# Optimization experiments

Measured on AMD Instinct MI355X. Metric: run time of the kernel, lower is better.

The kernel has to match this reference:

```python
import jax, jax.numpy as jnp
import numpy as np

BN_EPS = 1e-5


def _bn_relu(x, gamma, beta):
    # BatchNorm1d in train mode over (batch, spatial) per channel, then ReLU.
    mean = jnp.mean(x, axis=(0, 2), keepdims=True)
    var = jnp.var(x, axis=(0, 2), keepdims=True)
    xn = (x - mean) * jax.lax.rsqrt(var + BN_EPS)
    return jax.nn.relu(xn * gamma[None, :, None] + beta[None, :, None])


def setup_inputs() -> dict:
    key = jax.random.key(0)
    ks = jax.random.split(key, 12)
    B, d1, d2, n_p, n_g = 16, 128, 256, 8192, 2048
    d_cat, d_h, d_out = d1 + d2, 256, 128
    return {
        "feature1": jax.random.normal(ks[0], (B, d1, n_p), jnp.float32),
        "coord1": jax.random.normal(ks[1], (B, 3, n_p), jnp.float32),
        "feature2": jax.random.normal(ks[2], (B, d2, n_g), jnp.float32),
        "coord2": jax.random.normal(ks[3], (B, 3, n_g), jnp.float32),
        "W1": jax.random.normal(ks[4], (d_h, d_cat), jnp.float32) * 0.05,
        "b1": jax.random.normal(ks[5], (d_h,), jnp.float32) * 0.05,
        "gamma1": jnp.ones((d_h,), jnp.float32),
        "beta1": jnp.zeros((d_h,), jnp.float32),
        "W2": jax.random.normal(ks[6], (d_out, d_h), jnp.float32) * 0.05,
        "b2": jax.random.normal(ks[7], (d_out,), jnp.float32) * 0.05,
        "gamma2": jnp.ones((d_out,), jnp.float32),
        "beta2": jnp.zeros((d_out,), jnp.float32),
    }


def reference(feature1, coord1, feature2, coord2,
              W1, b1, gamma1, beta1, W2, b2, gamma2, beta2):
    c1 = coord1.transpose(0, 2, 1)      # [B, n_p, 3]
    c2 = coord2.transpose(0, 2, 1)      # [B, n_g, 3]
    f2 = feature2.transpose(0, 2, 1)    # [B, n_g, d2]

    # squared pairwise distances [B, n_p, n_g]
    d2sq = (jnp.sum(c1 * c1, -1)[:, :, None]
            + jnp.sum(c2 * c2, -1)[:, None, :]
            - 2.0 * jnp.einsum('bpd,bgd->bpg', c1, c2))

    # 3 nearest neighbors via top_k of negated distances (ascending distance)
    neg, idx = jax.lax.top_k(-d2sq, 3)
    dists = -neg                                     # [B, n_p, 3]
    recip = 1.0 / (dists + 1e-8)
    weight = recip / jnp.sum(recip, axis=-1, keepdims=True)

    gathered = jax.vmap(lambda f, i: f[i])(f2, idx)  # [B, n_p, 3, d2]
    interp = jnp.sum(gathered * weight[..., None], axis=2)  # [B, n_p, d2]

    feat = jnp.concatenate([feature1.transpose(0, 2, 1), interp], axis=-1)
    feat = feat.transpose(0, 2, 1)                   # [B, d1+d2, n_p]

    h = _bn_relu(jnp.einsum('oc,bcn->bon', W1, feat) + b1[None, :, None], gamma1, beta1)
    out = _bn_relu(jnp.einsum('oc,bcn->bon', W2, h) + b2[None, :, None], gamma2, beta2)
    return out
```

## Files before the change

kernel.cpp:

```cpp
#include <hip/hip_runtime.h>

#define BB   16
#define D1   128
#define D2   256
#define NP   8192
#define NG   2048
#define DC   384
#define DH   256
#define DO   128
#define NPTS (BB*NP)
#define KRANGE 4
#define KSLICE (NG/KRANGE)

typedef unsigned int u32;
typedef unsigned short u16;
typedef short v8s __attribute__((ext_vector_type(8)));
typedef float v4f __attribute__((ext_vector_type(4)));

__device__ __forceinline__ u16 f2bf(float f) {
  u32 u = __builtin_bit_cast(u32, f);
  return (u16)((u + 0x7FFFu + ((u >> 16) & 1u)) >> 16);
}
__device__ __forceinline__ float bf2f(u32 lo16) {
  return __builtin_bit_cast(float, lo16 << 16);
}

__device__ __forceinline__ void gload16(const void* g, void* s) {
  __builtin_amdgcn_global_load_lds((const __attribute__((address_space(1))) void*)g,
                                   (__attribute__((address_space(3))) void*)s, 16, 0, 0);
}

__global__ __launch_bounds__(256) void prepw_kernel(const float* __restrict__ W1,
                                                    const float* __restrict__ W2,
                                                    u16* __restrict__ W1s, u16* __restrict__ W2s) {
  int id = blockIdx.x * 256 + threadIdx.x;
  if (id < 12288) {
    int ks = id >> 11, rem = id & 2047, m = rem >> 3, blk = rem & 7;
    int k = ks * 64 + (blk ^ (m & 7)) * 8;
    const float* src = W1 + m * 384 + k;
    u32 a0 = (u32)f2bf(src[0]) | ((u32)f2bf(src[1]) << 16);
    u32 a1 = (u32)f2bf(src[2]) | ((u32)f2bf(src[3]) << 16);
    u32 a2 = (u32)f2bf(src[4]) | ((u32)f2bf(src[5]) << 16);
    u32 a3 = (u32)f2bf(src[6]) | ((u32)f2bf(src[7]) << 16);
    uint4 v; v.x=a0; v.y=a1; v.z=a2; v.w=a3;
    *(uint4*)((char*)W1s + (long)id * 16) = v;
  }
  int id2 = id - 12288;
  if (id2 >= 0 && id2 < 4096) {
    int ks = id2 >> 10, rem = id2 & 1023, m = rem >> 3, blk = rem & 7;
    int k = ks * 64 + (blk ^ (m & 7)) * 8;
    const float* src = W2 + m * 256 + k;
    u32 a0 = (u32)f2bf(src[0]) | ((u32)f2bf(src[1]) << 16);
    u32 a1 = (u32)f2bf(src[2]) | ((u32)f2bf(src[3]) << 16);
    u32 a2 = (u32)f2bf(src[4]) | ((u32)f2bf(src[5]) << 16);
    u32 a3 = (u32)f2bf(src[6]) | ((u32)f2bf(src[7]) << 16);
    uint4 v; v.x=a0; v.y=a1; v.z=a2; v.w=a3;
    *(uint4*)((char*)W2s + (long)id2 * 16) = v;
  }
}

__global__ __launch_bounds__(256) void tf2_kernel(const float* __restrict__ f2, u16* __restrict__ f2t) {
  __shared__ float tl[64 * 65];
  int b = blockIdx.z, t = threadIdx.x;
  int c0 = blockIdx.y * 64, g0 = blockIdx.x * 64;
  const float* src = f2 + ((long)b * 256 + c0) * 2048 + g0;
  for (int i = t; i < 4096; i += 256) {
    int c = i >> 6, g = i & 63;
    tl[c * 65 + g] = src[(long)c * 2048 + g];
  }
  __syncthreads();
  for (int i = t; i < 2048; i += 256) {
    int g = i >> 5, cp = i & 31;
    int c = cp * 2;
    u32 v = (u32)f2bf(tl[c * 65 + g]) | ((u32)f2bf(tl[(c + 1) * 65 + g]) << 16);
    *(u32*)((char*)f2t + (((long)b * 2048 + g0 + g) * 256 + c0 + c) * 2) = v;
  }
}

__global__ __launch_bounds__(256) void knn_part_kernel(const float* __restrict__ c1, const float* __restrict__ c2,
                                                       float* __restrict__ ktD, int* __restrict__ ktI) {
  __shared__ float4 sg[KSLICE];
  int b = blockIdx.z, r = blockIdx.y, t = threadIdx.x;
  int base = r * KSLICE;
  const float* c2b = c2 + (long)b * 3 * NG;
  for (int g = t; g < KSLICE; g += 256) {
    int gg = base + g;
    float x = c2b[gg], y = c2b[NG + gg], z = c2b[2 * NG + gg];
    float s2 = __fadd_rn(__fadd_rn(__fmul_rn(x, x), __fmul_rn(y, y)), __fmul_rn(z, z));
    sg[g] = make_float4(x, y, z, s2);
  }
  __syncthreads();
  int p = blockIdx.x * 256 + t;
  const float* c1b = c1 + (long)b * 3 * NP;
  float px = c1b[p], py = c1b[NP + p], pz = c1b[2 * NP + p];
  float s1 = __fadd_rn(__fadd_rn(__fmul_rn(px, px), __fmul_rn(py, py)), __fmul_rn(pz, pz));
  float t0 = 1e30f, t1 = 1e30f, t2v = 1e30f;
  int i0 = 0, i1 = 0, i2 = 0;
  for (int g0 = 0; g0 < KSLICE; g0 += 8) {
    u32 mask = 0;
    #pragma unroll
    for (int u = 0; u < 8; u++) {
      float4 q = sg[g0 + u];
      float dot = __fadd_rn(__fadd_rn(__fmul_rn(px, q.x), __fmul_rn(py, q.y)), __fmul_rn(pz, q.z));
      float du = __fsub_rn(__fadd_rn(s1, q.w), __fmul_rn(2.0f, dot));
      mask |= (du < t2v) ? (1u << u) : 0u;
    }
    while (mask) {
      int u = __builtin_ctz(mask);
      mask &= mask - 1;
      float4 q = sg[g0 + u];
      float dot = __fadd_rn(__fadd_rn(__fmul_rn(px, q.x), __fmul_rn(py, q.y)), __fmul_rn(pz, q.z));
      float dd = __fsub_rn(__fadd_rn(s1, q.w), __fmul_rn(2.0f, dot));
      if (dd < t2v) {
        int gi = base + g0 + u;
        if (dd < t1) {
          t2v = t1; i2 = i1;
          if (dd < t0) { t1 = t0; i1 = i0; t0 = dd; i0 = gi; }
          else         { t1 = dd; i1 = gi; }
        } else { t2v = dd; i2 = gi; }
      }
    }
  }
  long n = (long)b * NP + p;
  long o = (long)(r * 3) * NPTS + n;
  ktD[o] = t0; ktD[o + NPTS] = t1; ktD[o + 2 * (long)NPTS] = t2v;
  ktI[o] = i0; ktI[o + NPTS] = i1; ktI[o + 2 * (long)NPTS] = i2;
}

__global__ __launch_bounds__(256) void knn_merge_kernel(const float* __restrict__ ktD, const int* __restrict__ ktI,
                                                        int* __restrict__ ki, float* __restrict__ kw) {
  long n = (long)blockIdx.x * 256 + threadIdx.x;
  float t0 = 1e30f, t1 = 1e30f, t2v = 1e30f;
  int i0 = 0, i1 = 0, i2 = 0;
  #pragma unroll
  for (int e = 0; e < KRANGE * 3; e++) {
    float d = ktD[(long)e * NPTS + n];
    int gi = ktI[(long)e * NPTS + n];
    if (d < t2v) {
      if (d < t1) {
        t2v = t1; i2 = i1;
        if (d < t0) { t1 = t0; i1 = i0; t0 = d; i0 = gi; }
        else        { t1 = d;  i1 = gi; }
      } else { t2v = d; i2 = gi; }
    }
  }
  float r0 = __fdiv_rn(1.0f, __fadd_rn(t0, 1e-8f));
  float r1 = __fdiv_rn(1.0f, __fadd_rn(t1, 1e-8f));
  float r2 = __fdiv_rn(1.0f, __fadd_rn(t2v, 1e-8f));
  float rs = __fadd_rn(__fadd_rn(r0, r1), r2);
  long o = n * 3;
  ki[o] = i0; ki[o + 1] = i1; ki[o + 2] = i2;
  kw[o]     = __fdiv_rn(r0, rs);
  kw[o + 1] = __fdiv_rn(r1, rs);
  kw[o + 2] = __fdiv_rn(r2, rs);
}

__global__ __launch_bounds__(256) void interp_kernel(const float* __restrict__ f1, const u16* __restrict__ f2t,
                                                     const int* __restrict__ ki, const float* __restrict__ kw,
                                                     u16* __restrict__ feat) {
  __shared__ float tile[64 * 130];
  int b = blockIdx.y, t = threadIdx.x;
  long p0 = (long)blockIdx.x * 64;
  const float* f1b = f1 + (long)b * D1 * NP;
  for (int i = t; i < D1 * 64; i += 256) {
    int c = i >> 6, p = i & 63;
    tile[p * 130 + c] = f1b[(long)c * NP + p0 + p];
  }
  __syncthreads();
  int p = t >> 2, q = t & 3;
  long n = (long)b * NP + p0 + p;
  char* row = (char*)feat + n * 768;
  int sw = p & 7;
  #pragma unroll
  for (int g = 0; g < 4; g++) {
    int c = q * 32 + g * 8;
    u32 w0 = (u32)f2bf(tile[p*130 + c+0]) | ((u32)f2bf(tile[p*130 + c+1]) << 16);
    u32 w1 = (u32)f2bf(tile[p*130 + c+2]) | ((u32)f2bf(tile[p*130 + c+3]) << 16);
    u32 w2 = (u32)f2bf(tile[p*130 + c+4]) | ((u32)f2bf(tile[p*130 + c+5]) << 16);
    u32 w3 = (u32)f2bf(tile[p*130 + c+6]) | ((u32)f2bf(tile[p*130 + c+7]) << 16);
    uint4 v; v.x=w0; v.y=w1; v.z=w2; v.w=w3;
    int c6 = c >> 6, kblk = (c & 63) >> 3;
    *(uint4*)(row + c6 * 128 + ((kblk ^ sw) << 4)) = v;
  }
  long o = n * 3;
  int g0 = ki[o], g1 = ki[o + 1], g2 = ki[o + 2];
  float w0 = kw[o], w1 = kw[o + 1], w2 = kw[o + 2];
  const char* fb = (const char*)f2t + (long)b * NG * 512;
  const char* r0 = fb + (long)g0 * 512;
  const char* r1 = fb + (long)g1 * 512;
  const char* r2 = fb + (long)g2 * 512;
  #pragma unroll
  for (int g = 0; g < 8; g++) {
    int ci = q * 64 + g * 8;
    uint4 a0 = *(const uint4*)(r0 + ci * 2);
    uint4 a1 = *(const uint4*)(r1 + ci * 2);
    uint4 a2 = *(const uint4*)(r2 + ci * 2);
    const u32* pa0 = (const u32*)&a0;
    const u32* pa1 = (const u32*)&a1;
    const u32* pa2 = (const u32*)&a2;
    u32 outw[4];
    #pragma unroll
    for (int h = 0; h < 4; h++) {
      u32 x0 = pa0[h], x1 = pa1[h], x2 = pa2[h];
      float lo = w0 * bf2f(x0 & 0xffff) + w1 * bf2f(x1 & 0xffff) + w2 * bf2f(x2 & 0xffff);
      float hi = w0 * bf2f(x0 >> 16)    + w1 * bf2f(x1 >> 16)    + w2 * bf2f(x2 >> 16);
      outw[h] = (u32)f2bf(lo) | ((u32)f2bf(hi) << 16);
    }
    uint4 v; v.x=outw[0]; v.y=outw[1]; v.z=outw[2]; v.w=outw[3];
    int c = 128 + ci;
    int c6 = c >> 6, kblk = (c & 63) >> 3;
    *(uint4*)(row + c6 * 128 + ((kblk ^ sw) << 4)) = v;
  }
}

__device__ __forceinline__ void mfma_tile(const char* lds, int buf, int wm, int wn, int l, v4f acc[4][4]) {
  const char* A = lds + buf * 16384;
  const char* Bp = lds + 32768 + buf * 16384;
  int lm = l & 15, lk = l >> 4, l7 = l & 7;
  #pragma unroll
  for (int w32 = 0; w32 < 2; w32++) {
    v8s af[4], bfr[4];
    #pragma unroll
    for (int mf = 0; mf < 4; mf++)
      af[mf] = *(const v8s*)(A + (wm * 64 + mf * 16 + lm) * 128 + (((w32 * 4 + lk) ^ l7) << 4));
    #pragma unroll
    for (int nf = 0; nf < 4; nf++)
      bfr[nf] = *(const v8s*)(Bp + (wn * 64 + nf * 16 + lm) * 128 + (((w32 * 4 + lk) ^ l7) << 4));
    #pragma unroll
    for (int mf = 0; mf < 4; mf++)
      #pragma unroll
      for (int nf = 0; nf < 4; nf++)
        acc[mf][nf] = __builtin_amdgcn_mfma_f32_16x16x32_bf16(af[mf], bfr[nf], acc[mf][nf], 0, 0, 0);
  }
}

__global__ __launch_bounds__(256) void gemm1_kernel(const u16* __restrict__ W1s, const u16* __restrict__ feat,
                                                    const float* __restrict__ b1, u16* __restrict__ y1,
                                                    float* __restrict__ ps, float* __restrict__ pq) {
  __shared__ __attribute__((aligned(16))) char lds[65536];
  const int t = threadIdx.x, w = t >> 6, l = t & 63;
  const int wm = w >> 1, wn = w & 1;
  const int nb = blockIdx.y, mb = blockIdx.x;
  const long n0 = (long)nb * 128;
  const int m0 = mb * 128;
  v4f acc[4][4];
  #pragma unroll
  for (int i = 0; i < 4; i++)
    #pragma unroll
    for (int j = 0; j < 4; j++) { v4f z = {0.f,0.f,0.f,0.f}; acc[i][j] = z; }

  auto stage = [&](int ks, int buf) {
    const char* srcA = (const char*)W1s + ks * 32768 + (long)m0 * 128 + w * 4096 + l * 16;
    char* dstA = (char*)lds + buf * 16384 + w * 4096;
    #pragma unroll
    for (int i = 0; i < 4; i++) gload16(srcA + i * 1024, dstA + i * 1024);
    char* dstB = (char*)lds + 32768 + buf * 16384 + w * 4096;
    #pragma unroll
    for (int i = 0; i < 4; i++) {
      int a = w * 4096 + i * 1024 + l * 16;
      int n = a >> 7, r = a & 127;
      const char* srcB = (const char*)feat + (n0 + n) * 768 + ks * 128 + r;
      gload16(srcB, dstB + i * 1024);
    }
  };

  stage(0, 0);
  __syncthreads();
  int buf = 0;
  for (int ks = 0; ks < 6; ks++) {
    if (ks < 5) stage(ks + 1, buf ^ 1);
    mfma_tile(lds, buf, wm, wn, l, acc);
    __syncthreads();
    buf ^= 1;
  }

  const int lm = l & 15, lk = l >> 4;
  #pragma unroll
  for (int mf = 0; mf < 4; mf++) {
    int m = m0 + wm * 64 + mf * 16 + lk * 4;
    float bb0 = b1[m], bb1 = b1[m+1], bb2 = b1[m+2], bb3 = b1[m+3];
    #pragma unroll
    for (int nf = 0; nf < 4; nf++) {
      long n = n0 + wn * 64 + nf * 16 + lm;
      v4f v = acc[mf][nf];
      v[0] += bb0; v[1] += bb1; v[2] += bb2; v[3] += bb3;
      acc[mf][nf] = v;
      uint2 pk;
      pk.x = (u32)f2bf(v[0]) | ((u32)f2bf(v[1]) << 16);
      pk.y = (u32)f2bf(v[2]) | ((u32)f2bf(v[3]) << 16);
      *(uint2*)((char*)y1 + (n * 256 + m) * 2) = pk;
    }
  }
  #pragma unroll
  for (int mf = 0; mf < 4; mf++) {
    #pragma unroll
    for (int j = 0; j < 4; j++) {
      float s = 0.f, q = 0.f;
      #pragma unroll
      for (int nf = 0; nf < 4; nf++) { float v = acc[mf][nf][j]; s += v; q += v * v; }
      #pragma unroll
      for (int mask = 1; mask <= 8; mask <<= 1) { s += __shfl_xor(s, mask); q += __shfl_xor(q, mask); }
      if (lm == 0) {
        int m = m0 + wm * 64 + mf * 16 + lk * 4 + j;
        int col = nb * 2 + wn;
        ps[(long)m * 2048 + col] = s;
        pq[(long)m * 2048 + col] = q;
      }
    }
  }
}

__global__ __launch_bounds__(256) void stats_kernel(const float* __restrict__ ps, const float* __restrict__ pq,
                                                    const float* __restrict__ gamma, const float* __restrict__ beta,
                                                    float* __restrict__ scsh, int ncols, float invN) {
  int m = blockIdx.x, t = threadIdx.x;
  float s = 0.f, q = 0.f;
  for (int i = t; i < ncols; i += 256) { s += ps[(long)m * ncols + i]; q += pq[(long)m * ncols + i]; }
  __shared__ float rs[4], rq[4];
  #pragma unroll
  for (int mask = 1; mask <= 32; mask <<= 1) { s += __shfl_xor(s, mask); q += __shfl_xor(q, mask); }
  int w = t >> 6;
  if ((t & 63) == 0) { rs[w] = s; rq[w] = q; }
  __syncthreads();
  if (t == 0) {
    s = rs[0] + rs[1] + rs[2] + rs[3];
    q = rq[0] + rq[1] + rq[2] + rq[3];
    float mean = s * invN;
    float var = q * invN - mean * mean;
    float rstd = rsqrtf(var + 1e-5f);
    float sc = gamma[m] * rstd;
    scsh[m] = sc;
    scsh[gridDim.x + m] = beta[m] - mean * sc;
  }
}

__global__ __launch_bounds__(256) void gemm2_kernel(const u16* __restrict__ W2s, const u16* __restrict__ y1,
                                                    const float* __restrict__ scsh, const float* __restrict__ b2,
                                                    u16* __restrict__ y2, float* __restrict__ ps, float* __restrict__ pq) {
  __shared__ __attribute__((aligned(16))) char lds[65536];
  const int t = threadIdx.x, w = t >> 6, l = t & 63;
  const int wm = w >> 1, wn = w & 1;
  const int nb = blockIdx.x;
  const long n0 = (long)nb * 128;
  v4f acc[4][4];
  #pragma unroll
  for (int i = 0; i < 4; i++)
    #pragma unroll
    for (int j = 0; j < 4; j++) { v4f z = {0.f,0.f,0.f,0.f}; acc[i][j] = z; }
  uint4 breg[4];

  auto stageA = [&](int ks, int buf) {
    const char* src = (const char*)W2s + ks * 16384 + w * 4096 + l * 16;
    char* dst = (char*)lds + buf * 16384 + w * 4096;
    #pragma unroll
    for (int i = 0; i < 4; i++) gload16(src + i * 1024, dst + i * 1024);
  };
  auto loadB = [&](int ks) {
    #pragma unroll
    for (int i = 0; i < 4; i++) {
      int idx = i * 256 + t, n = idx >> 3, blk = idx & 7;
      breg[i] = *(const uint4*)((const char*)y1 + (n0 + n) * 512 + ks * 128 + blk * 16);
    }
  };
  auto writeB = [&](int ks, int buf) {
    #pragma unroll
    for (int i = 0; i < 4; i++) {
      int idx = i * 256 + t, n = idx >> 3, blk = idx & 7;
      const u32* pr = (const u32*)&breg[i];
      u32 outw[4];
      #pragma unroll
      for (int h = 0; h < 4; h++) {
        int k = ks * 64 + blk * 8 + 2 * h;
        u32 x = pr[h];
        float h0 = fmaxf(0.f, scsh[k]     * bf2f(x & 0xffff) + scsh[256 + k]);
        float h1 = fmaxf(0.f, scsh[k + 1] * bf2f(x >> 16)    + scsh[256 + k + 1]);
        outw[h] = (u32)f2bf(h0) | ((u32)f2bf(h1) << 16);
      }
      uint4 v; v.x=outw[0]; v.y=outw[1]; v.z=outw[2]; v.w=outw[3];
      *(uint4*)((char*)lds + 32768 + buf * 16384 + n * 128 + ((blk ^ (n & 7)) << 4)) = v;
    }
  };

  stageA(0, 0); loadB(0); writeB(0, 0);
  __syncthreads();
  int buf = 0;
  for (int ks = 0; ks < 4; ks++) {
    if (ks < 3) { stageA(ks + 1, buf ^ 1); loadB(ks + 1); }
    mfma_tile(lds, buf, wm, wn, l, acc);
    if (ks < 3) writeB(ks + 1, buf ^ 1);
    __syncthreads();
    buf ^= 1;
  }

  const int lm = l & 15, lk = l >> 4;
  #pragma unroll
  for (int mf = 0; mf < 4; mf++) {
    int m = wm * 64 + mf * 16 + lk * 4;
    float bb0 = b2[m], bb1 = b2[m+1], bb2v = b2[m+2], bb3 = b2[m+3];
    #pragma unroll
    for (int nf = 0; nf < 4; nf++) {
      long n = n0 + wn * 64 + nf * 16 + lm;
      v4f v = acc[mf][nf];
      v[0] += bb0; v[1] += bb1; v[2] += bb2v; v[3] += bb3;
      acc[mf][nf] = v;
      uint2 pk;
      pk.x = (u32)f2bf(v[0]) | ((u32)f2bf(v[1]) << 16);
      pk.y = (u32)f2bf(v[2]) | ((u32)f2bf(v[3]) << 16);
      *(uint2*)((char*)y2 + (n * 128 + m) * 2) = pk;
    }
  }
  #pragma unroll
  for (int mf = 0; mf < 4; mf++) {
    #pragma unroll
    for (int j = 0; j < 4; j++) {
      float s = 0.f, q = 0.f;
      #pragma unroll
      for (int nf = 0; nf < 4; nf++) { float v = acc[mf][nf][j]; s += v; q += v * v; }
      #pragma unroll
      for (int mask = 1; mask <= 8; mask <<= 1) { s += __shfl_xor(s, mask); q += __shfl_xor(q, mask); }
      if (lm == 0) {
        int m = wm * 64 + mf * 16 + lk * 4 + j;
        int col = nb * 2 + wn;
        ps[(long)m * 2048 + col] = s;
        pq[(long)m * 2048 + col] = q;
      }
    }
  }
}

__global__ __launch_bounds__(256) void final_kernel(const u16* __restrict__ y2, const float* __restrict__ scsh2,
                                                    float* __restrict__ out) {
  __shared__ float tl[64 * 130];
  __shared__ float sc[128], sh[128];
  int b = blockIdx.y, t = threadIdx.x;
  long p0 = (long)blockIdx.x * 64;
  if (t < 128) { sc[t] = scsh2[t]; sh[t] = scsh2[128 + t]; }
  __syncthreads();
  #pragma unroll
  for (int i = 0; i < 4; i++) {
    int idx = i * 256 + t;
    int n = idx >> 4, cb = idx & 15;
    uint4 v = *(const uint4*)((const char*)y2 + (((long)b * NP + p0 + n) * 128 + cb * 8) * 2);
    const u32* pv = (const u32*)&v;
    #pragma unroll
    for (int h = 0; h < 4; h++) {
      int m = cb * 8 + 2 * h;
      u32 x = pv[h];
      tl[n * 130 + m]     = fmaxf(0.f, sc[m]     * bf2f(x & 0xffff) + sh[m]);
      tl[n * 130 + m + 1] = fmaxf(0.f, sc[m + 1] * bf2f(x >> 16)    + sh[m + 1]);
    }
  }
  __syncthreads();
  int m = t & 127, hh = t >> 7;
  float* dst = out + ((long)b * 128 + m) * NP + p0 + hh * 32;
  #pragma unroll
  for (int j = 0; j < 8; j++) {
    int p = hh * 32 + j * 4;
    float4 v;
    v.x = tl[(p + 0) * 130 + m];
    v.y = tl[(p + 1) * 130 + m];
    v.z = tl[(p + 2) * 130 + m];
    v.w = tl[(p + 3) * 130 + m];
    *(float4*)(dst + j * 4) = v;
  }
}

extern "C" void kernel_launch(void* const* d_in, const int* in_sizes, int n_in,
                              void* d_out, int out_size, void* d_ws, size_t ws_size,
                              hipStream_t stream) {
  const float* f1  = (const float*)d_in[0];
  const float* c1  = (const float*)d_in[1];
  const float* f2  = (const float*)d_in[2];
  const float* c2  = (const float*)d_in[3];
  const float* W1  = (const float*)d_in[4];
  const float* b1  = (const float*)d_in[5];
  const float* g1  = (const float*)d_in[6];
  const float* be1 = (const float*)d_in[7];
  const float* W2  = (const float*)d_in[8];
  const float* b2  = (const float*)d_in[9];
  const float* g2  = (const float*)d_in[10];
  const float* be2 = (const float*)d_in[11];
  float* out = (float*)d_out;

  char* ws = (char*)d_ws;
  size_t off = 0;
  auto alloc = [&](size_t sz) { char* p = ws + off; off = (off + sz + 255) & ~(size_t)255; return p; };
  u16*   f2t   = (u16*)  alloc((size_t)BB * NG * D2 * 2);
  u16*   W1s   = (u16*)  alloc(196608);
  u16*   W2s   = (u16*)  alloc(65536);
  int*   ki    = (int*)  alloc((size_t)NPTS * 3 * 4);
  float* kw    = (float*)alloc((size_t)NPTS * 3 * 4);
  float* ps1   = (float*)alloc((size_t)256 * 2048 * 4);
  float* pq1   = (float*)alloc((size_t)256 * 2048 * 4);
  float* scsh1 = (float*)alloc(2048);
  float* ps2   = (float*)alloc((size_t)128 * 2048 * 4);
  float* pq2   = (float*)alloc((size_t)128 * 2048 * 4);
  float* scsh2 = (float*)alloc(1024);
  u16*   y1    = (u16*)  alloc((size_t)NPTS * DH * 2);
  u16*   feat  = (u16*)  alloc((size_t)NPTS * DC * 2);
  u16*   y2    = (u16*)  feat;

  float* ktD = (float*)y1;
  int*   ktI = (int*)((char*)y1 + (size_t)KRANGE * 3 * NPTS * 4 + 256);

  hipLaunchKernelGGL(prepw_kernel, dim3(64), dim3(256), 0, stream, W1, W2, W1s, W2s);
  hipLaunchKernelGGL(tf2_kernel, dim3(NG / 64, D2 / 64, BB), dim3(256), 0, stream, f2, f2t);
  hipLaunchKernelGGL(knn_part_kernel, dim3(NP / 256, KRANGE, BB), dim3(256), 0, stream, c1, c2, ktD, ktI);
  hipLaunchKernelGGL(knn_merge_kernel, dim3(NPTS / 256), dim3(256), 0, stream, ktD, ktI, ki, kw);
  hipLaunchKernelGGL(interp_kernel, dim3(NP / 64, BB), dim3(256), 0, stream, f1, f2t, ki, kw, feat);
  hipLaunchKernelGGL(gemm1_kernel, dim3(2, NPTS / 128), dim3(256), 0, stream, W1s, feat, b1, y1, ps1, pq1);
  hipLaunchKernelGGL(stats_kernel, dim3(256), dim3(256), 0, stream, ps1, pq1, g1, be1, scsh1, 2048, 1.f / (float)NPTS);
  hipLaunchKernelGGL(gemm2_kernel, dim3(NPTS / 128), dim3(256), 0, stream, W2s, y1, scsh1, b2, y2, ps2, pq2);
  hipLaunchKernelGGL(stats_kernel, dim3(128), dim3(256), 0, stream, ps2, pq2, g2, be2, scsh2, 2048, 1.f / (float)NPTS);
  hipLaunchKernelGGL(final_kernel, dim3(NP / 64, BB), dim3(256), 0, stream, y2, scsh2, out);
}
```

Before: 354.7 us.

## Fuse KNN merge into interp kernel and make top-3 insertion branchless

The separate knn_merge kernel is removed. Its merge of the partial top-3 candidates and the inverse-distance weight computation now run inside interp_kernel, which reads ktD/ktI directly. This drops one launch and the ki/kw round trip through global memory. The top-3 insertion in knn_part uses fmed3/fmin and selects instead of nested branches to cut divergence. The single part launch is split into two launches over the ranges, which adds launch overhead and looks like an experiment.

Measured after the change: 361.7 us. No clear change (+2.0%).

```diff
diff --git a/kernel.cpp b/kernel.cpp
--- a/kernel.cpp
+++ b/kernel.cpp
@@ -78,9 +78,9 @@
 }
 
 __global__ __launch_bounds__(256) void knn_part_kernel(const float* __restrict__ c1, const float* __restrict__ c2,
-                                                       float* __restrict__ ktD, int* __restrict__ ktI) {
+                                                       float* __restrict__ ktD, int* __restrict__ ktI, int rbase) {
   __shared__ float4 sg[KSLICE];
-  int b = blockIdx.z, r = blockIdx.y, t = threadIdx.x;
+  int b = blockIdx.z, r = rbase + blockIdx.y, t = threadIdx.x;
   int base = r * KSLICE;
   const float* c2b = c2 + (long)b * 3 * NG;
   for (int g = t; g < KSLICE; g += 256) {
@@ -111,14 +111,16 @@
       float4 q = sg[g0 + u];
       float dot = __fadd_rn(__fadd_rn(__fmul_rn(px, q.x), __fmul_rn(py, q.y)), __fmul_rn(pz, q.z));
       float dd = __fsub_rn(__fadd_rn(s1, q.w), __fmul_rn(2.0f, dot));
-      if (dd < t2v) {
-        int gi = base + g0 + u;
-        if (dd < t1) {
-          t2v = t1; i2 = i1;
-          if (dd < t0) { t1 = t0; i1 = i0; t0 = dd; i0 = gi; }
-          else         { t1 = dd; i1 = gi; }
-        } else { t2v = dd; i2 = gi; }
-      }
+      int gi = base + g0 + u;
+      bool c0 = dd < t0, cc1 = dd < t1, cc2 = dd < t2v;
+      int ni2 = cc1 ? i1 : (cc2 ? gi : i2);
+      int ni1 = c0 ? i0 : (cc1 ? gi : i1);
+      int ni0 = c0 ? gi : i0;
+      float nt2 = __builtin_amdgcn_fmed3f(t1, dd, t2v);
+      float nt1 = __builtin_amdgcn_fmed3f(t0, dd, t1);
+      float nt0 = fminf(t0, dd);
+      t0 = nt0; t1 = nt1; t2v = nt2;
+      i0 = ni0; i1 = ni1; i2 = ni2;
     }
   }
   long n = (long)b * NP + p;
@@ -127,9 +129,33 @@
   ktI[o] = i0; ktI[o + NPTS] = i1; ktI[o + 2 * (long)NPTS] = i2;
 }
 
-__global__ __launch_bounds__(256) void knn_merge_kernel(const float* __restrict__ ktD, const int* __restrict__ ktI,
-                                                        int* __restrict__ ki, float* __restrict__ kw) {
-  long n = (long)blockIdx.x * 256 + threadIdx.x;
+__global__ __launch_bounds__(256) void interp_kernel(const float* __restrict__ f1, const u16* __restrict__ f2t,
+                                                     const float* __restrict__ ktD, const int* __restrict__ ktI,
+                                                     u16* __restrict__ feat) {
+  __shared__ float tile[64 * 130];
+  int b = blockIdx.y, t = threadIdx.x;
+  long p0 = (long)blockIdx.x * 64;
+  const float* f1b = f1 + (long)b * D1 * NP;
+  for (int i = t; i < D1 * 64; i += 256) {
+    int c = i >> 6, p = i & 63;
+    tile[p * 130 + c] = f1b[(long)c * NP + p0 + p];
+  }
+  __syncthreads();
+  int p = t >> 2, q = t & 3;
+  long n = (long)b * NP + p0 + p;
+  char* row = (char*)feat + n * 768;
+  int sw = p & 7;
+  #pragma unroll
+  for (int g = 0; g < 4; g++) {
+    int c = q * 32 + g * 8;
+    u32 w0 = (u32)f2bf(tile[p*130 + c+0]) | ((u32)f2bf(tile[p*130 + c+1]) << 16);
+    u32 w1 = (u32)f2bf(tile[p*130 + c+2]) | ((u32)f2bf(tile[p*130 + c+3]) << 16);
+    u32 w2 = (u32)f2bf(tile[p*130 + c+4]) | ((u32)f2bf(tile[p*130 + c+5]) << 16);
+    u32 w3 = (u32)f2bf(tile[p*130 + c+6]) | ((u32)f2bf(tile[p*130 + c+7]) << 16);
+    uint4 v; v.x=w0; v.y=w1; v.z=w2; v.w=w3;
+    int c6 = c >> 6, kblk = (c & 63) >> 3;
+    *(uint4*)(row + c6 * 128 + ((kblk ^ sw) << 4)) = v;
+  }
   float t0 = 1e30f, t1 = 1e30f, t2v = 1e30f;
   int i0 = 0, i1 = 0, i2 = 0;
   #pragma unroll
@@ -144,51 +170,17 @@
       } else { t2v = d; i2 = gi; }
     }
   }
-  float r0 = __fdiv_rn(1.0f, __fadd_rn(t0, 1e-8f));
-  float r1 = __fdiv_rn(1.0f, __fadd_rn(t1, 1e-8f));
-  float r2 = __fdiv_rn(1.0f, __fadd_rn(t2v, 1e-8f));
-  float rs = __fadd_rn(__fadd_rn(r0, r1), r2);
-  long o = n * 3;
-  ki[o] = i0; ki[o + 1] = i1; ki[o + 2] = i2;
-  kw[o]     = __fdiv_rn(r0, rs);
-  kw[o + 1] = __fdiv_rn(r1, rs);
-  kw[o + 2] = __fdiv_rn(r2, rs);
-}
-
-__global__ __launch_bounds__(256) void interp_kernel(const float* __restrict__ f1, const u16* __restrict__ f2t,
-                                                     const int* __restrict__ ki, const float* __restrict__ kw,
-                                                     u16* __restrict__ feat) {
-  __shared__ float tile[64 * 130];
-  int b = blockIdx.y, t = threadIdx.x;
-  long p0 = (long)blockIdx.x * 64;
-  const float* f1b = f1 + (long)b * D1 * NP;
-  for (int i = t; i < D1 * 64; i += 256) {
-    int c = i >> 6, p = i & 63;
-    tile[p * 130 + c] = f1b[(long)c * NP + p0 + p];
-  }
-  __syncthreads();
-  int p = t >> 2, q = t & 3;
-  long n = (long)b * NP + p0 + p;
-  char* row = (char*)feat + n * 768;
-  int sw = p & 7;
-  #pragma unroll
-  for (int g = 0; g < 4; g++) {
-    int c = q * 32 + g * 8;
-    u32 w0 = (u32)f2bf(tile[p*130 + c+0]) | ((u32)f2bf(tile[p*130 + c+1]) << 16);
-    u32 w1 = (u32)f2bf(tile[p*130 + c+2]) | ((u32)f2bf(tile[p*130 + c+3]) << 16);
-    u32 w2 = (u32)f2bf(tile[p*130 + c+4]) | ((u32)f2bf(tile[p*130 + c+5]) << 16);
-    u32 w3 = (u32)f2bf(tile[p*130 + c+6]) | ((u32)f2bf(tile[p*130 + c+7]) << 16);
-    uint4 v; v.x=w0; v.y=w1; v.z=w2; v.w=w3;
-    int c6 = c >> 6, kblk = (c & 63) >> 3;
-    *(uint4*)(row + c6 * 128 + ((kblk ^ sw) << 4)) = v;
-  }
-  long o = n * 3;
-  int g0 = ki[o], g1 = ki[o + 1], g2 = ki[o + 2];
-  float w0 = kw[o], w1 = kw[o + 1], w2 = kw[o + 2];
+  float rr0 = __fdiv_rn(1.0f, __fadd_rn(t0, 1e-8f));
+  float rr1 = __fdiv_rn(1.0f, __fadd_rn(t1, 1e-8f));
+  float rr2 = __fdiv_rn(1.0f, __fadd_rn(t2v, 1e-8f));
+  float rs = __fadd_rn(__fadd_rn(rr0, rr1), rr2);
+  float w0 = __fdiv_rn(rr0, rs);
+  float w1 = __fdiv_rn(rr1, rs);
+  float w2 = __fdiv_rn(rr2, rs);
   const char* fb = (const char*)f2t + (long)b * NG * 512;
-  const char* r0 = fb + (long)g0 * 512;
-  const char* r1 = fb + (long)g1 * 512;
-  const char* r2 = fb + (long)g2 * 512;
+  const char* r0 = fb + (long)i0 * 512;
+  const char* r1 = fb + (long)i1 * 512;
+  const char* r2 = fb + (long)i2 * 512;
   #pragma unroll
   for (int g = 0; g < 8; g++) {
     int ci = q * 64 + g * 8;
@@ -488,8 +480,6 @@
   u16*   f2t   = (u16*)  alloc((size_t)BB * NG * D2 * 2);
   u16*   W1s   = (u16*)  alloc(196608);
   u16*   W2s   = (u16*)  alloc(65536);
-  int*   ki    = (int*)  alloc((size_t)NPTS * 3 * 4);
-  float* kw    = (float*)alloc((size_t)NPTS * 3 * 4);
   float* ps1   = (float*)alloc((size_t)256 * 2048 * 4);
   float* pq1   = (float*)alloc((size_t)256 * 2048 * 4);
   float* scsh1 = (float*)alloc(2048);
@@ -505,9 +495,9 @@
 
   hipLaunchKernelGGL(prepw_kernel, dim3(64), dim3(256), 0, stream, W1, W2, W1s, W2s);
   hipLaunchKernelGGL(tf2_kernel, dim3(NG / 64, D2 / 64, BB), dim3(256), 0, stream, f2, f2t);
-  hipLaunchKernelGGL(knn_part_kernel, dim3(NP / 256, KRANGE, BB), dim3(256), 0, stream, c1, c2, ktD, ktI);
-  hipLaunchKernelGGL(knn_merge_kernel, dim3(NPTS / 256), dim3(256), 0, stream, ktD, ktI, ki, kw);
-  hipLaunchKernelGGL(interp_kernel, dim3(NP / 64, BB), dim3(256), 0, stream, f1, f2t, ki, kw, feat);
+  hipLaunchKernelGGL(knn_part_kernel, dim3(NP / 256, 2, BB), dim3(256), 0, stream, c1, c2, ktD, ktI, 0);
+  hipLaunchKernelGGL(knn_part_kernel, dim3(NP / 256, 2, BB), dim3(256), 0, stream, c1, c2, ktD, ktI, 2);
+  hipLaunchKernelGGL(interp_kernel, dim3(NP / 64, BB), dim3(256), 0, stream, f1, f2t, ktD, ktI, feat);
   hipLaunchKernelGGL(gemm1_kernel, dim3(2, NPTS / 128), dim3(256), 0, stream, W1s, feat, b1, y1, ps1, pq1);
   hipLaunchKernelGGL(stats_kernel, dim3(256), dim3(256), 0, stream, ps1, pq1, g1, be1, scsh1, 2048, 1.f / (float)NPTS);
   hipLaunchKernelGGL(gemm2_kernel, dim3(NPTS / 128), dim3(256), 0, stream, W2s, y1, scsh1, b2, y2, ps2, pq2);
```
